# Optimization experiments

Measured on AMD Instinct MI355X. Metric: run time of the kernel, lower is better.

Reference implementation:

```python
import jax, jax.numpy as jnp
import numpy as np

N_HEAD, M_DIM, K_DIM, V_DIM = 16, 1024, 64, 64
LN_EPS = 1e-5


def setup_inputs() -> dict:
    key = jax.random.key(0)
    ks = jax.random.split(key, 10)
    B, L = 4, 2048
    q = jax.random.normal(ks[0], (B, L, M_DIM), dtype=jnp.float32)
    k = jax.random.normal(ks[1], (B, L, M_DIM), dtype=jnp.float32)
    v = jax.random.normal(ks[2], (B, L, M_DIM), dtype=jnp.float32)
    s = 1.0 / np.sqrt(M_DIM)
    W_qs = jax.random.normal(ks[3], (M_DIM, N_HEAD * K_DIM), dtype=jnp.float32) * s
    W_ks = jax.random.normal(ks[4], (M_DIM, N_HEAD * K_DIM), dtype=jnp.float32) * s
    W_vs = jax.random.normal(ks[5], (M_DIM, N_HEAD * V_DIM), dtype=jnp.float32) * s
    fc_w = jax.random.normal(ks[6], (N_HEAD * V_DIM, M_DIM), dtype=jnp.float32) * (1.0 / np.sqrt(N_HEAD * V_DIM))
    fc_b = jnp.zeros((M_DIM,), dtype=jnp.float32)
    ln_g = jnp.ones((M_DIM,), dtype=jnp.float32)
    ln_b = jnp.zeros((M_DIM,), dtype=jnp.float32)
    return {"q": q, "k": k, "v": v, "W_qs": W_qs, "W_ks": W_ks, "W_vs": W_vs,
            "fc_w": fc_w, "fc_b": fc_b, "ln_g": ln_g, "ln_b": ln_b}


def reference(q, k, v, W_qs, W_ks, W_vs, fc_w, fc_b, ln_g, ln_b):
    B, Lq, _ = q.shape
    residual = q
    # project and split heads: [B, L, H, D]
    qh = (q @ W_qs).reshape(B, Lq, N_HEAD, K_DIM)
    kh = (k @ W_ks).reshape(B, k.shape[1], N_HEAD, K_DIM)
    vh = (v @ W_vs).reshape(B, v.shape[1], N_HEAD, V_DIM)
    temperature = np.power(K_DIM, 0.5).astype(np.float32)
    # attention scores [B, H, Lq, Lk]
    attn = jnp.einsum('bqhd,bkhd->bhqk', qh, kh) / temperature
    attn = jax.nn.softmax(attn, axis=-1)
    out = jnp.einsum('bhqk,bkhd->bqhd', attn, vh).reshape(B, Lq, N_HEAD * V_DIM)
    out = out @ fc_w + fc_b
    x = out + residual
    mu = jnp.mean(x, axis=-1, keepdims=True)
    var = jnp.mean(jnp.square(x - mu), axis=-1, keepdims=True)
    return (x - mu) * jax.lax.rsqrt(var + LN_EPS) * ln_g + ln_b
```

## Files before the change

### kernel.cpp

```cpp
#include <hip/hip_runtime.h>
#include <math.h>

#define NHEAD 16
#define MDIM  1024
#define KD    64
#define BATCH 4
#define SEQ   2048
#define MROWS (BATCH*SEQ)

using short8 = __attribute__((ext_vector_type(8))) short;
using f4     = __attribute__((ext_vector_type(4))) float;

__device__ inline short f2bf(float x) {
  union { float f; unsigned u; } v; v.f = x;
  unsigned r = v.u + 0x7fffu + ((v.u >> 16) & 1u);
  return (short)(r >> 16);
}

__device__ __forceinline__ float fast_exp2(float x) {
#if __has_builtin(__builtin_amdgcn_exp2f)
  return __builtin_amdgcn_exp2f(x);
#else
  return exp2f(x);
#endif
}

__device__ __forceinline__ int pack_bf16(float lo, float hi) {
#if __has_builtin(__builtin_amdgcn_cvt_pk_bf16_f32)
  auto t = __builtin_amdgcn_cvt_pk_bf16_f32(lo, hi);
  int r; __builtin_memcpy(&r, &t, 4); return r;
#else
  unsigned u0 = __float_as_uint(lo) + 0x8000u;
  unsigned u1 = __float_as_uint(hi) + 0x8000u;
  return (int)__builtin_amdgcn_perm(u1, u0, 0x07060302u);
#endif
}

__device__ __forceinline__ void g2l16(const void* g, void* l) {
  __builtin_amdgcn_global_load_lds((const __attribute__((address_space(1))) unsigned int*)g,
                                   (__attribute__((address_space(3))) unsigned int*)l, 16, 0, 0);
}

__global__ void wtrans_kernel(const float* __restrict__ w0, const float* __restrict__ w1,
                              const float* __restrict__ w2, const float* __restrict__ w3,
                              short* __restrict__ o0, short* __restrict__ o1,
                              short* __restrict__ o2, short* __restrict__ o3) {
  int z = blockIdx.z;
  const float* in = z == 0 ? w0 : (z == 1 ? w1 : (z == 2 ? w2 : w3));
  short* out = z == 0 ? o0 : (z == 1 ? o1 : (z == 2 ? o2 : o3));
  __shared__ float t[32][33];
  int bx = blockIdx.x * 32, by = blockIdx.y * 32;
  int tx = threadIdx.x, ty = threadIdx.y;
#pragma unroll
  for (int i = 0; i < 4; i++)
    t[ty + i * 8][tx] = in[(size_t)(by + ty + i * 8) * MDIM + bx + tx];
  __syncthreads();
#pragma unroll
  for (int i = 0; i < 4; i++)
    out[(size_t)(bx + ty + i * 8) * MDIM + by + tx] = f2bf(t[tx][ty + i * 8]);
}

__global__ void cvt_kernel(const float* __restrict__ q, const float* __restrict__ k,
                           const float* __restrict__ v, short* __restrict__ qb,
                           short* __restrict__ kb, short* __restrict__ vb) {
  const float* in = blockIdx.y == 0 ? q : (blockIdx.y == 1 ? k : v);
  short* out = blockIdx.y == 0 ? qb : (blockIdx.y == 1 ? kb : vb);
  size_t i = (size_t)blockIdx.x * 256 + threadIdx.x;
  float4 a = ((const float4*)in)[2 * i];
  float4 b = ((const float4*)in)[2 * i + 1];
  short8 s = {f2bf(a.x), f2bf(a.y), f2bf(a.z), f2bf(a.w),
              f2bf(b.x), f2bf(b.y), f2bf(b.z), f2bf(b.w)};
  ((short8*)out)[i] = s;
}

#define GEMM_STAGE_SETUP(Ab, Bt)                                                   \
  int srow = lane >> 2;                                                            \
  int sch = (lane & 3) ^ (srow & 3);                                               \
  const short* aSrc0 = Ab + (size_t)(m0 + wave * 32 + srow) * 1024 + sch * 8;      \
  const short* aSrc1 = aSrc0 + (size_t)16 * 1024;                                  \
  const short* bSrc0 = Bt + (size_t)(n0 + wave * 32 + srow) * 1024 + sch * 8;      \
  const short* bSrc1 = bSrc0 + (size_t)16 * 1024;

#define GEMM_MAIN_LOOP()                                                           \
  auto stage = [&](int k0, int b) {                                                \
    g2l16(aSrc0 + k0, &As[b][wave * 1024]);                                        \
    g2l16(aSrc1 + k0, &As[b][wave * 1024 + 512]);                                  \
    g2l16(bSrc0 + k0, &Bs[b][wave * 1024]);                                        \
    g2l16(bSrc1 + k0, &Bs[b][wave * 1024 + 512]);                                  \
  };                                                                               \
  stage(0, 0);                                                                     \
  __syncthreads();                                                                 \
  int aoff = (quad ^ (low & 3)) * 8;                                               \
  for (int k0 = 0; k0 < 1024; k0 += 32) {                                          \
    int b = (k0 >> 5) & 1;                                                         \
    if (k0 + 32 < 1024) stage(k0 + 32, b ^ 1);                                     \
    short8 af[4], bfr[4];                                                          \
    _Pragma("unroll")                                                              \
    for (int m = 0; m < 4; m++) af[m] = *(const short8*)&As[b][(wr + m * 16 + low) * 32 + aoff]; \
    _Pragma("unroll")                                                              \
    for (int n = 0; n < 4; n++) bfr[n] = *(const short8*)&Bs[b][(wc + n * 16 + low) * 32 + aoff]; \
    _Pragma("unroll")                                                              \
    for (int m = 0; m < 4; m++)                                                    \
      _Pragma("unroll")                                                            \
      for (int n = 0; n < 4; n++)                                                  \
        acc[m][n] = __builtin_amdgcn_mfma_f32_16x16x32_bf16(af[m], bfr[n], acc[m][n], 0, 0, 0); \
    __syncthreads();                                                               \
  }

__launch_bounds__(256, 4)
__global__ void gemm_qkv_kernel(const short* __restrict__ qb, const short* __restrict__ kb,
                                const short* __restrict__ vb, const short* __restrict__ Wqt,
                                const short* __restrict__ Wkt, const short* __restrict__ Wvt,
                                short* __restrict__ Qh, short* __restrict__ Kh,
                                short* __restrict__ Vt) {
  __shared__ __attribute__((aligned(16))) short As[2][128 * 32];
  __shared__ __attribute__((aligned(16))) short Bs[2][128 * 32];
  int z = blockIdx.z;
  const short* Ab = z == 0 ? qb : (z == 1 ? kb : vb);
  const short* Bt = z == 0 ? Wqt : (z == 1 ? Wkt : Wvt);
  int tid = threadIdx.x, wave = tid >> 6, lane = tid & 63;
  int quad = lane >> 4, low = lane & 15;
  int m0 = blockIdx.x * 128, n0 = blockIdx.y * 128;
  int wr = (wave >> 1) * 64, wc = (wave & 1) * 64;

  GEMM_STAGE_SETUP(Ab, Bt)

  f4 acc[4][4];
#pragma unroll
  for (int m = 0; m < 4; m++)
#pragma unroll
    for (int n = 0; n < 4; n++) { acc[m][n][0] = 0.f; acc[m][n][1] = 0.f; acc[m][n][2] = 0.f; acc[m][n][3] = 0.f; }

  GEMM_MAIN_LOOP()

  float scale = z == 0 ? 0.18033688011112042f : 1.0f;
  short* dst = z == 0 ? Qh : (z == 1 ? Kh : Vt);
#pragma unroll
  for (int m = 0; m < 4; m++)
#pragma unroll
    for (int n = 0; n < 4; n++)
#pragma unroll
      for (int r2 = 0; r2 < 4; r2++) {
        int gr = m0 + wr + m * 16 + quad * 4 + r2;
        int gc = n0 + wc + n * 16 + low;
        float val = acc[m][n][r2];
        int b = gr >> 11, l = gr & 2047, h = gc >> 6, d = gc & 63;
        if (z < 2)
          dst[(((size_t)(b * NHEAD + h)) * SEQ + l) * KD + d] = f2bf(val * scale);
        else
          dst[(((size_t)(b * NHEAD + h)) * KD + d) * SEQ + l] = f2bf(val);
      }
}

__launch_bounds__(256, 4)
__global__ void gemm_fc_kernel(const short* __restrict__ Ab, const short* __restrict__ Bt,
                               float* __restrict__ dst, const float* __restrict__ bias,
                               const float* __restrict__ res) {
  __shared__ __attribute__((aligned(16))) short As[2][128 * 32];
  __shared__ __attribute__((aligned(16))) short Bs[2][128 * 32];
  int tid = threadIdx.x, wave = tid >> 6, lane = tid & 63;
  int quad = lane >> 4, low = lane & 15;
  int m0 = blockIdx.x * 128, n0 = blockIdx.y * 128;
  int wr = (wave >> 1) * 64, wc = (wave & 1) * 64;

  GEMM_STAGE_SETUP(Ab, Bt)

  f4 acc[4][4];
#pragma unroll
  for (int m = 0; m < 4; m++)
#pragma unroll
    for (int n = 0; n < 4; n++) { acc[m][n][0] = 0.f; acc[m][n][1] = 0.f; acc[m][n][2] = 0.f; acc[m][n][3] = 0.f; }

  GEMM_MAIN_LOOP()

#pragma unroll
  for (int m = 0; m < 4; m++)
#pragma unroll
    for (int n = 0; n < 4; n++)
#pragma unroll
      for (int r2 = 0; r2 < 4; r2++) {
        int gr = m0 + wr + m * 16 + quad * 4 + r2;
        int gc = n0 + wc + n * 16 + low;
        dst[(size_t)gr * 1024 + gc] = acc[m][n][r2] + bias[gc] + res[(size_t)gr * 1024 + gc];
      }
}

__launch_bounds__(256, 3)
__global__ void attn_kernel(const short* __restrict__ Qh, const short* __restrict__ Kh,
                            const short* __restrict__ Vt, short* __restrict__ Out) {
  __shared__ __attribute__((aligned(16))) short KT[2][64 * 64];
  __shared__ __attribute__((aligned(16))) short VT[2][64 * 64];
  __shared__ __attribute__((aligned(16))) short Ps[4][32 * 72];
  int tid = threadIdx.x;
  int wave = tid >> 6, lane = tid & 63, quad = lane >> 4, low = lane & 15;
  int bh = blockIdx.y;
  int q0 = blockIdx.x * 128 + wave * 32;

  const short* Qb = Qh + (size_t)bh * SEQ * KD;
  const short* Kb = Kh + (size_t)bh * SEQ * KD;
  const short* Vb = Vt + (size_t)bh * KD * SEQ;
  short* Pw = &Ps[wave][0];

  int srow = lane >> 3;
  int sch = (lane & 7) ^ srow;
  const short* kSrc0 = Kb + (size_t)(wave * 16 + srow) * KD + sch * 8;
  const short* kSrc1 = kSrc0 + (size_t)8 * KD;
  const short* vSrc0 = Vb + (size_t)(wave * 16 + srow) * SEQ + sch * 8;
  const short* vSrc1 = vSrc0 + (size_t)8 * SEQ;

  auto stage = [&](int k0, int b) {
    g2l16(kSrc0 + (size_t)k0 * KD, &KT[b][wave * 1024]);
    g2l16(kSrc1 + (size_t)k0 * KD, &KT[b][wave * 1024 + 512]);
    g2l16(vSrc0 + k0, &VT[b][wave * 1024]);
    g2l16(vSrc1 + k0, &VT[b][wave * 1024 + 512]);
  };

  short8 qf[2][2];
#pragma unroll
  for (int qt = 0; qt < 2; qt++)
#pragma unroll
    for (int h = 0; h < 2; h++)
      qf[qt][h] = *(const short8*)&Qb[(size_t)(q0 + qt * 16 + low) * KD + h * 32 + quad * 8];

  f4 Oacc[2][4], lacc[2];
#pragma unroll
  for (int qt = 0; qt < 2; qt++) {
    lacc[qt][0] = 0.f; lacc[qt][1] = 0.f; lacc[qt][2] = 0.f; lacc[qt][3] = 0.f;
#pragma unroll
    for (int nt = 0; nt < 4; nt++) { Oacc[qt][nt][0] = 0.f; Oacc[qt][nt][1] = 0.f; Oacc[qt][nt][2] = 0.f; Oacc[qt][nt][3] = 0.f; }
  }
  const f4 fzero = {0.f, 0.f, 0.f, 0.f};
  const short8 onesb = {0x3F80, 0x3F80, 0x3F80, 0x3F80, 0x3F80, 0x3F80, 0x3F80, 0x3F80};

  stage(0, 0);
  __syncthreads();

  for (int c = 0; c < SEQ / 64; c++) {
    int b = c & 1;
    if (c + 1 < SEQ / 64) stage((c + 1) * 64, b ^ 1);

    short8 kf[4][2];
#pragma unroll
    for (int nt = 0; nt < 4; nt++)
#pragma unroll
      for (int h = 0; h < 2; h++)
        kf[nt][h] = *(const short8*)&KT[b][(nt * 16 + low) * 64 + ((h * 4 + quad) ^ (low & 7)) * 8];

#pragma unroll
    for (int qt = 0; qt < 2; qt++) {
      f4 S[4];
#pragma unroll
      for (int nt = 0; nt < 4; nt++) {
        S[nt] = __builtin_amdgcn_mfma_f32_16x16x32_bf16(kf[nt][0], qf[qt][0], fzero, 0, 0, 0);
        S[nt] = __builtin_amdgcn_mfma_f32_16x16x32_bf16(kf[nt][1], qf[qt][1], S[nt], 0, 0, 0);
      }
#pragma unroll
      for (int nt = 0; nt < 4; nt++) {
        int2 pk;
        pk.x = pack_bf16(fast_exp2(S[nt][0]), fast_exp2(S[nt][1]));
        pk.y = pack_bf16(fast_exp2(S[nt][2]), fast_exp2(S[nt][3]));
        *(int2*)&Pw[(qt * 16 + low) * 72 + nt * 16 + quad * 4] = pk;
      }
    }

    short8 pf[2][2];
#pragma unroll
    for (int qt = 0; qt < 2; qt++)
#pragma unroll
      for (int h = 0; h < 2; h++)
        pf[qt][h] = *(const short8*)&Pw[(qt * 16 + low) * 72 + h * 32 + quad * 8];

#pragma unroll
    for (int qt = 0; qt < 2; qt++) {
      lacc[qt] = __builtin_amdgcn_mfma_f32_16x16x32_bf16(pf[qt][0], onesb, lacc[qt], 0, 0, 0);
      lacc[qt] = __builtin_amdgcn_mfma_f32_16x16x32_bf16(pf[qt][1], onesb, lacc[qt], 0, 0, 0);
    }

#pragma unroll
    for (int nt = 0; nt < 4; nt++) {
      short8 vf0 = *(const short8*)&VT[b][(nt * 16 + low) * 64 + ((quad) ^ (low & 7)) * 8];
      short8 vf1 = *(const short8*)&VT[b][(nt * 16 + low) * 64 + ((4 + quad) ^ (low & 7)) * 8];
#pragma unroll
      for (int qt = 0; qt < 2; qt++) {
        Oacc[qt][nt] = __builtin_amdgcn_mfma_f32_16x16x32_bf16(pf[qt][0], vf0, Oacc[qt][nt], 0, 0, 0);
        Oacc[qt][nt] = __builtin_amdgcn_mfma_f32_16x16x32_bf16(pf[qt][1], vf1, Oacc[qt][nt], 0, 0, 0);
      }
    }
    __syncthreads();
  }

  int b = bh >> 4, h = bh & 15;
#pragma unroll
  for (int qt = 0; qt < 2; qt++)
#pragma unroll
    for (int r = 0; r < 4; r++) {
      float iv = 1.0f / lacc[qt][r];
#pragma unroll
      for (int nt = 0; nt < 4; nt++) {
        size_t idx = ((size_t)(b * SEQ + q0 + qt * 16 + quad * 4 + r)) * 1024 + h * 64 + nt * 16 + low;
        Out[idx] = f2bf(Oacc[qt][nt][r] * iv);
      }
    }
}

__launch_bounds__(256)
__global__ void ln_kernel(const float* __restrict__ x, const float* __restrict__ g,
                          const float* __restrict__ b, float* __restrict__ out) {
  int row = blockIdx.x, tid = threadIdx.x;
  const float4* xr = (const float4*)(x + (size_t)row * 1024);
  float4 v = xr[tid];
  float s = v.x + v.y + v.z + v.w;
  float q = v.x * v.x + v.y * v.y + v.z * v.z + v.w * v.w;
#pragma unroll
  for (int o = 32; o > 0; o >>= 1) { s += __shfl_xor(s, o); q += __shfl_xor(q, o); }
  __shared__ float ss[4], sq[4];
  if ((tid & 63) == 0) { ss[tid >> 6] = s; sq[tid >> 6] = q; }
  __syncthreads();
  if (tid == 0) {
    float S = ss[0] + ss[1] + ss[2] + ss[3];
    float Q = sq[0] + sq[1] + sq[2] + sq[3];
    float mean = S * (1.f / 1024.f);
    float var = Q * (1.f / 1024.f) - mean * mean;
    ss[0] = mean; sq[0] = rsqrtf(var + 1e-5f);
  }
  __syncthreads();
  float mean = ss[0], rs = sq[0];
  const float4* g4 = (const float4*)g;
  const float4* b4 = (const float4*)b;
  float4 gg = g4[tid], bb = b4[tid], o;
  o.x = (v.x - mean) * rs * gg.x + bb.x;
  o.y = (v.y - mean) * rs * gg.y + bb.y;
  o.z = (v.z - mean) * rs * gg.z + bb.z;
  o.w = (v.w - mean) * rs * gg.w + bb.w;
  ((float4*)(out + (size_t)row * 1024))[tid] = o;
}

extern "C" void kernel_launch(void* const* d_in, const int* in_sizes, int n_in,
                              void* d_out, int out_size, void* d_ws, size_t ws_size,
                              hipStream_t stream) {
  const float* q   = (const float*)d_in[0];
  const float* k   = (const float*)d_in[1];
  const float* v   = (const float*)d_in[2];
  const float* Wq  = (const float*)d_in[3];
  const float* Wk  = (const float*)d_in[4];
  const float* Wv  = (const float*)d_in[5];
  const float* fcw = (const float*)d_in[6];
  const float* fcb = (const float*)d_in[7];
  const float* lng = (const float*)d_in[8];
  const float* lnb = (const float*)d_in[9];
  float* out = (float*)d_out;

  char* ws = (char*)d_ws;
  const size_t MB = 1024 * 1024;
  short* Wqt = (short*)(ws + 0 * MB);
  short* Wkt = (short*)(ws + 2 * MB);
  short* Wvt = (short*)(ws + 4 * MB);
  short* fct = (short*)(ws + 6 * MB);
  short* qb  = (short*)(ws + 8 * MB);
  short* kb  = (short*)(ws + 24 * MB);
  short* vb  = (short*)(ws + 40 * MB);
  short* Kh  = (short*)(ws + 8 * MB);
  short* Vt  = (short*)(ws + 24 * MB);
  short* Ao  = (short*)(ws + 40 * MB);
  short* Qh  = (short*)(ws + 56 * MB);
  float* X   = (float*)(ws + 8 * MB);

  wtrans_kernel<<<dim3(32, 32, 4), dim3(32, 8), 0, stream>>>(Wq, Wk, Wv, fcw, Wqt, Wkt, Wvt, fct);

  cvt_kernel<<<dim3(MROWS * MDIM / 8 / 256, 3), 256, 0, stream>>>(q, k, v, qb, kb, vb);

  gemm_qkv_kernel<<<dim3(64, 8, 3), 256, 0, stream>>>(qb, kb, vb, Wqt, Wkt, Wvt, Qh, Kh, Vt);

  attn_kernel<<<dim3(SEQ / 128, BATCH * NHEAD), 256, 0, stream>>>(Qh, Kh, Vt, Ao);

  gemm_fc_kernel<<<dim3(64, 8), 256, 0, stream>>>(Ao, fct, X, fcb, q);

  ln_kernel<<<MROWS, 256, 0, stream>>>(X, lng, lnb, out);
}
```

Measured before the change: 377.9 us.

## Switch attention to 32x32 MFMA and keep P in registers via permlane swap

The attention kernel moves from 16x16x32 to 32x32x16 bf16 MFMA tiles. The exponentiated scores are rearranged into the A-operand layout with v_permlane32_swap instead of a round trip through per-wave shared memory, which removes the Ps buffer and its LDS traffic. The change also adds s_setprio around the MFMA bursts and raises the occupancy hint in launch bounds from 3 to 4. The larger accumulators (three 16-float vectors) raise register pressure, and the fixed row and column mapping has to match the MFMA layout exactly.

Result: no change. 377.3 us (-0.2%).

```diff
diff --git a/kernel.cpp b/kernel.cpp
--- a/kernel.cpp
+++ b/kernel.cpp
@@ -10,6 +10,7 @@
 
 using short8 = __attribute__((ext_vector_type(8))) short;
 using f4     = __attribute__((ext_vector_type(4))) float;
+using f16x   = __attribute__((ext_vector_type(16))) float;
 
 __device__ inline short f2bf(float x) {
   union { float f; unsigned u; } v; v.f = x;
@@ -185,21 +186,20 @@
       }
 }
 
-__launch_bounds__(256, 3)
+__launch_bounds__(256, 4)
 __global__ void attn_kernel(const short* __restrict__ Qh, const short* __restrict__ Kh,
                             const short* __restrict__ Vt, short* __restrict__ Out) {
   __shared__ __attribute__((aligned(16))) short KT[2][64 * 64];
   __shared__ __attribute__((aligned(16))) short VT[2][64 * 64];
-  __shared__ __attribute__((aligned(16))) short Ps[4][32 * 72];
   int tid = threadIdx.x;
-  int wave = tid >> 6, lane = tid & 63, quad = lane >> 4, low = lane & 15;
+  int wave = tid >> 6, lane = tid & 63;
+  int l = lane & 31, hi = lane >> 5;
   int bh = blockIdx.y;
   int q0 = blockIdx.x * 128 + wave * 32;
 
   const short* Qb = Qh + (size_t)bh * SEQ * KD;
   const short* Kb = Kh + (size_t)bh * SEQ * KD;
   const short* Vb = Vt + (size_t)bh * KD * SEQ;
-  short* Pw = &Ps[wave][0];
 
   int srow = lane >> 3;
   int sch = (lane & 7) ^ srow;
@@ -215,21 +215,14 @@
     g2l16(vSrc1 + k0, &VT[b][wave * 1024 + 512]);
   };
 
-  short8 qf[2][2];
-#pragma unroll
-  for (int qt = 0; qt < 2; qt++)
-#pragma unroll
-    for (int h = 0; h < 2; h++)
-      qf[qt][h] = *(const short8*)&Qb[(size_t)(q0 + qt * 16 + low) * KD + h * 32 + quad * 8];
-
-  f4 Oacc[2][4], lacc[2];
-#pragma unroll
-  for (int qt = 0; qt < 2; qt++) {
-    lacc[qt][0] = 0.f; lacc[qt][1] = 0.f; lacc[qt][2] = 0.f; lacc[qt][3] = 0.f;
-#pragma unroll
-    for (int nt = 0; nt < 4; nt++) { Oacc[qt][nt][0] = 0.f; Oacc[qt][nt][1] = 0.f; Oacc[qt][nt][2] = 0.f; Oacc[qt][nt][3] = 0.f; }
-  }
-  const f4 fzero = {0.f, 0.f, 0.f, 0.f};
+  short8 qf[4];
+#pragma unroll
+  for (int ks = 0; ks < 4; ks++)
+    qf[ks] = *(const short8*)&Qb[(size_t)(q0 + l) * KD + ks * 16 + hi * 8];
+
+  f16x Oacc[2], lacc;
+#pragma unroll
+  for (int i = 0; i < 16; i++) { Oacc[0][i] = 0.f; Oacc[1][i] = 0.f; lacc[i] = 0.f; }
   const short8 onesb = {0x3F80, 0x3F80, 0x3F80, 0x3F80, 0x3F80, 0x3F80, 0x3F80, 0x3F80};
 
   stage(0, 0);
@@ -239,68 +232,65 @@
     int b = c & 1;
     if (c + 1 < SEQ / 64) stage((c + 1) * 64, b ^ 1);
 
-    short8 kf[4][2];
-#pragma unroll
-    for (int nt = 0; nt < 4; nt++)
-#pragma unroll
-      for (int h = 0; h < 2; h++)
-        kf[nt][h] = *(const short8*)&KT[b][(nt * 16 + low) * 64 + ((h * 4 + quad) ^ (low & 7)) * 8];
-
-#pragma unroll
-    for (int qt = 0; qt < 2; qt++) {
-      f4 S[4];
-#pragma unroll
-      for (int nt = 0; nt < 4; nt++) {
-        S[nt] = __builtin_amdgcn_mfma_f32_16x16x32_bf16(kf[nt][0], qf[qt][0], fzero, 0, 0, 0);
-        S[nt] = __builtin_amdgcn_mfma_f32_16x16x32_bf16(kf[nt][1], qf[qt][1], S[nt], 0, 0, 0);
+#pragma unroll
+    for (int nt = 0; nt < 2; nt++) {
+      short8 kf[4];
+#pragma unroll
+      for (int ks = 0; ks < 4; ks++)
+        kf[ks] = *(const short8*)&KT[b][(nt * 32 + l) * 64 + (((ks * 2 + hi) ^ (l & 7)) * 8)];
+
+      f16x S;
+#pragma unroll
+      for (int i = 0; i < 16; i++) S[i] = 0.f;
+      __builtin_amdgcn_s_setprio(1);
+#pragma unroll
+      for (int ks = 0; ks < 4; ks++)
+        S = __builtin_amdgcn_mfma_f32_32x32x16_bf16(kf[ks], qf[ks], S, 0, 0, 0);
+      __builtin_amdgcn_s_setprio(0);
+
+      int u[8];
+#pragma unroll
+      for (int i = 0; i < 8; i++)
+        u[i] = pack_bf16(fast_exp2(S[2 * i]), fast_exp2(S[2 * i + 1]));
+      asm("v_permlane32_swap_b32 %0, %1" : "+v"(u[0]), "+v"(u[2]));
+      asm("v_permlane32_swap_b32 %0, %1" : "+v"(u[1]), "+v"(u[3]));
+      asm("v_permlane32_swap_b32 %0, %1" : "+v"(u[4]), "+v"(u[6]));
+      asm("v_permlane32_swap_b32 %0, %1" : "+v"(u[5]), "+v"(u[7]));
+      short8 pa0, pa1;
+      {
+        int t0[4] = {u[0], u[1], u[2], u[3]};
+        int t1[4] = {u[4], u[5], u[6], u[7]};
+        __builtin_memcpy(&pa0, t0, 16);
+        __builtin_memcpy(&pa1, t1, 16);
       }
-#pragma unroll
-      for (int nt = 0; nt < 4; nt++) {
-        int2 pk;
-        pk.x = pack_bf16(fast_exp2(S[nt][0]), fast_exp2(S[nt][1]));
-        pk.y = pack_bf16(fast_exp2(S[nt][2]), fast_exp2(S[nt][3]));
-        *(int2*)&Pw[(qt * 16 + low) * 72 + nt * 16 + quad * 4] = pk;
+
+      __builtin_amdgcn_s_setprio(1);
+      lacc = __builtin_amdgcn_mfma_f32_32x32x16_bf16(pa0, onesb, lacc, 0, 0, 0);
+      lacc = __builtin_amdgcn_mfma_f32_32x32x16_bf16(pa1, onesb, lacc, 0, 0, 0);
+
+#pragma unroll
+      for (int dt = 0; dt < 2; dt++) {
+        short8 vf0 = *(const short8*)&VT[b][(dt * 32 + l) * 64 + (((nt * 4 + 0 + hi) ^ (l & 7)) * 8)];
+        short8 vf1 = *(const short8*)&VT[b][(dt * 32 + l) * 64 + (((nt * 4 + 2 + hi) ^ (l & 7)) * 8)];
+        Oacc[dt] = __builtin_amdgcn_mfma_f32_32x32x16_bf16(pa0, vf0, Oacc[dt], 0, 0, 0);
+        Oacc[dt] = __builtin_amdgcn_mfma_f32_32x32x16_bf16(pa1, vf1, Oacc[dt], 0, 0, 0);
       }
-    }
-
-    short8 pf[2][2];
-#pragma unroll
-    for (int qt = 0; qt < 2; qt++)
-#pragma unroll
-      for (int h = 0; h < 2; h++)
-        pf[qt][h] = *(const short8*)&Pw[(qt * 16 + low) * 72 + h * 32 + quad * 8];
-
-#pragma unroll
-    for (int qt = 0; qt < 2; qt++) {
-      lacc[qt] = __builtin_amdgcn_mfma_f32_16x16x32_bf16(pf[qt][0], onesb, lacc[qt], 0, 0, 0);
-      lacc[qt] = __builtin_amdgcn_mfma_f32_16x16x32_bf16(pf[qt][1], onesb, lacc[qt], 0, 0, 0);
-    }
-
-#pragma unroll
-    for (int nt = 0; nt < 4; nt++) {
-      short8 vf0 = *(const short8*)&VT[b][(nt * 16 + low) * 64 + ((quad) ^ (low & 7)) * 8];
-      short8 vf1 = *(const short8*)&VT[b][(nt * 16 + low) * 64 + ((4 + quad) ^ (low & 7)) * 8];
-#pragma unroll
-      for (int qt = 0; qt < 2; qt++) {
-        Oacc[qt][nt] = __builtin_amdgcn_mfma_f32_16x16x32_bf16(pf[qt][0], vf0, Oacc[qt][nt], 0, 0, 0);
-        Oacc[qt][nt] = __builtin_amdgcn_mfma_f32_16x16x32_bf16(pf[qt][1], vf1, Oacc[qt][nt], 0, 0, 0);
-      }
+      __builtin_amdgcn_s_setprio(0);
     }
     __syncthreads();
   }
 
-  int b = bh >> 4, h = bh & 15;
-#pragma unroll
-  for (int qt = 0; qt < 2; qt++)
-#pragma unroll
-    for (int r = 0; r < 4; r++) {
-      float iv = 1.0f / lacc[qt][r];
-#pragma unroll
-      for (int nt = 0; nt < 4; nt++) {
-        size_t idx = ((size_t)(b * SEQ + q0 + qt * 16 + quad * 4 + r)) * 1024 + h * 64 + nt * 16 + low;
-        Out[idx] = f2bf(Oacc[qt][nt][r] * iv);
-      }
+  int bb = bh >> 4, h = bh & 15;
+#pragma unroll
+  for (int r = 0; r < 16; r++) {
+    int qrow = q0 + (r & 3) + 8 * (r >> 2) + 4 * hi;
+    float iv = 1.0f / lacc[r];
+#pragma unroll
+    for (int dt = 0; dt < 2; dt++) {
+      size_t idx = ((size_t)(bb * SEQ + qrow)) * 1024 + h * 64 + dt * 32 + l;
+      Out[idx] = f2bf(Oacc[dt][r] * iv);
     }
+  }
 }
 
 __launch_bounds__(256)
```
